# Performance work log

Measured on AMD Instinct MI355X. Metric: run time of the kernel, lower is better.

## Reference

```python
import jax, jax.numpy as jnp
import numpy as np

H = 4          # number of GCN heads (hard-coded self.h = 4)
EPS = 1e-6     # MWPToolkit LayerNorm eps
B, K, D, HID = 16, 1024, 256, 256
DK = D // H


def setup_inputs() -> dict:
    key = jax.random.key(0)
    ks = jax.random.split(key, 12)
    sc = lambda fan_in: 1.0 / np.sqrt(fan_in).astype(np.float32)
    return {
        "graph_nodes": jax.random.normal(ks[0], (B, K, D), jnp.float32),
        "graph": jax.random.randint(ks[1], (B, 5, K, K), 0, 2, jnp.int32),
        # per-head GCN layer 1: GraphConvolution(indim -> hiddim)
        "Wg1": jax.random.normal(ks[2], (H, D, HID), jnp.float32) * sc(D),
        "bg1": jax.random.normal(ks[3], (H, HID), jnp.float32) * sc(D),
        # per-head GCN layer 2: GraphConvolution(hiddim -> d_k)
        "Wg2": jax.random.normal(ks[4], (H, HID, DK), jnp.float32) * sc(HID),
        "bg2": jax.random.normal(ks[5], (H, DK), jnp.float32) * sc(HID),
        # PositionwiseFeedForward: Linear(indim,hiddim) -> ReLU -> Linear(hiddim,outdim)
        "Wf1": jax.random.normal(ks[6], (D, HID), jnp.float32) * sc(D),
        "bf1": jax.random.normal(ks[7], (HID,), jnp.float32) * sc(D),
        "Wf2": jax.random.normal(ks[8], (HID, D), jnp.float32) * sc(HID),
        "bf2": jax.random.normal(ks[9], (D,), jnp.float32) * sc(HID),
        # LayerNorm(outdim) affine params
        "ln_a": jnp.ones((D,), jnp.float32),
        "ln_b": jnp.zeros((D,), jnp.float32),
    }


def reference(graph_nodes, graph, Wg1, bg1, Wg2, bg2, Wf1, bf1, Wf2, bf2, ln_a, ln_b):
    adj = graph.astype(jnp.float32)                      # (B, 5, K, K)
    # adj_list = [adj[:,1], adj[:,1], adj[:,4], adj[:,4]] -> stack heads
    adj_h = jnp.stack([adj[:, 1], adj[:, 1], adj[:, 4], adj[:, 4]])  # (H,B,K,K)

    # GCN layer 1 (all heads at once): relu(adj @ (x @ W1) + b1)
    sup1 = jnp.einsum('bkd,hdf->hbkf', graph_nodes, Wg1)            # (H,B,K,HID)
    h1 = jax.nn.relu(jnp.einsum('hbkj,hbjf->hbkf', adj_h, sup1)
                     + bg1[:, None, None, :])
    # (dropout is identity in eval)
    # GCN layer 2: adj @ (h1 @ W2) + b2
    sup2 = jnp.einsum('hbkf,hfe->hbke', h1, Wg2)                    # (H,B,K,DK)
    h2 = jnp.einsum('hbkj,hbje->hbke', adj_h, sup2) + bg2[:, None, None, :]

    # concat heads along feature dim: (B,K,H*DK) == (B,K,D)
    g = jnp.transpose(h2, (1, 2, 0, 3)).reshape(h2.shape[1], h2.shape[2], -1)

    # MWPToolkit LayerNorm: a*(x-mean)/(std+eps)+b, std unbiased (ddof=1)
    mu = g.mean(-1, keepdims=True)
    sd = jnp.std(g, axis=-1, keepdims=True, ddof=1)
    g = ln_a * (g - mu) / (sd + EPS) + ln_b + graph_nodes           # residual

    # PositionwiseFeedForward + residual (dropout identity in eval)
    ff = jax.nn.relu(g @ Wf1 + bf1) @ Wf2 + bf2
    out = ff + g
    return adj, out
```

## Files before the change

kernel.cpp:

```cpp
#include <hip/hip_runtime.h>

typedef unsigned short ushort_t;
using short8  = __attribute__((ext_vector_type(8))) short;
using floatx4 = __attribute__((ext_vector_type(4))) float;

__device__ __forceinline__ ushort_t f2bf(float f) {
  unsigned int x = __builtin_bit_cast(unsigned int, f);
  x += 0x7fffu + ((x >> 16) & 1u);
  return (ushort_t)(x >> 16);
}

__device__ __forceinline__ void gld16(const ushort_t* g, ushort_t* l) {
  __builtin_amdgcn_global_load_lds(
      (const __attribute__((address_space(1))) void*)(unsigned long long)(uintptr_t)g,
      (__attribute__((address_space(3))) void*)l, 16, 0, 0);
}

template <typename F>
__device__ __forceinline__ void gemm_tile(const ushort_t* __restrict__ A, int lda,
                                          const ushort_t* __restrict__ BT, int ldb,
                                          int K, F epi) {
  __shared__ ushort_t As[128 * 64];
  __shared__ ushort_t Bs[128 * 64];

  const int tid  = threadIdx.x;
  const int wave = tid >> 6;
  const int lane = tid & 63;
  const int l15  = lane & 15;
  const int quad = lane >> 4;
  const int wm   = wave >> 1;
  const int wn   = wave & 1;

  const int srow8  = lane >> 3;
  const int schunk = lane & 7;
  const int gcol   = ((schunk ^ srow8) * 8);

  const ushort_t* gA = A  + (size_t)(wave * 32 + srow8) * lda + gcol;
  const ushort_t* gB = BT + (size_t)(wave * 32 + srow8) * ldb + gcol;
  ushort_t* lA = As + (wave * 32) * 64;
  ushort_t* lB = Bs + (wave * 32) * 64;

  floatx4 acc[4][4] = {};
  const int arow0 = (wm * 64 + l15) * 64;
  const int brow0 = (wn * 64 + l15) * 64;
  const int cx    = l15 & 7;

  for (int k0 = 0; k0 < K; k0 += 64) {
#pragma unroll
    for (int ci = 0; ci < 4; ci++) {
      gld16(gA + (size_t)(ci * 8) * lda, lA + ci * 512);
      gld16(gB + (size_t)(ci * 8) * ldb, lB + ci * 512);
    }
    gA += 64; gB += 64;
    __syncthreads();
#pragma unroll
    for (int ks = 0; ks < 2; ks++) {
      const int cs = ((ks * 4 + quad) ^ cx) * 8;
      short8 af[4], bfr[4];
#pragma unroll
      for (int i = 0; i < 4; i++) af[i]  = *(const short8*)(As + arow0 + i * 1024 + cs);
#pragma unroll
      for (int j = 0; j < 4; j++) bfr[j] = *(const short8*)(Bs + brow0 + j * 1024 + cs);
#pragma unroll
      for (int i = 0; i < 4; i++)
#pragma unroll
        for (int j = 0; j < 4; j++)
          acc[i][j] = __builtin_amdgcn_mfma_f32_16x16x32_bf16(af[i], bfr[j], acc[i][j], 0, 0, 0);
    }
    __syncthreads();
  }

#pragma unroll
  for (int i = 0; i < 4; i++)
#pragma unroll
    for (int j = 0; j < 4; j++)
#pragma unroll
      for (int r = 0; r < 4; r++)
        epi(wm * 64 + i * 16 + quad * 4 + r, wn * 64 + j * 16 + l15, acc[i][j][r]);
}

template <typename F>
__device__ __forceinline__ void gemm_tile64(const ushort_t* __restrict__ A, int lda,
                                            const ushort_t* __restrict__ BT, int ldb,
                                            int K, F epi) {
  __shared__ ushort_t As[64 * 64];
  __shared__ ushort_t Bs[128 * 64];

  const int tid  = threadIdx.x;
  const int wave = tid >> 6;
  const int lane = tid & 63;
  const int l15  = lane & 15;
  const int quad = lane >> 4;
  const int wm   = wave >> 1;
  const int wn   = wave & 1;

  const int srow8  = lane >> 3;
  const int schunk = lane & 7;
  const int gcol   = ((schunk ^ srow8) * 8);

  const ushort_t* gA = A  + (size_t)(wave * 16 + srow8) * lda + gcol;
  const ushort_t* gB = BT + (size_t)(wave * 32 + srow8) * ldb + gcol;
  ushort_t* lA = As + (wave * 16) * 64;
  ushort_t* lB = Bs + (wave * 32) * 64;

  floatx4 acc[2][4] = {};
  const int arow0 = (wm * 32 + l15) * 64;
  const int brow0 = (wn * 64 + l15) * 64;
  const int cx    = l15 & 7;

  for (int k0 = 0; k0 < K; k0 += 64) {
#pragma unroll
    for (int ci = 0; ci < 2; ci++)
      gld16(gA + (size_t)(ci * 8) * lda, lA + ci * 512);
#pragma unroll
    for (int ci = 0; ci < 4; ci++)
      gld16(gB + (size_t)(ci * 8) * ldb, lB + ci * 512);
    gA += 64; gB += 64;
    __syncthreads();
#pragma unroll
    for (int ks = 0; ks < 2; ks++) {
      const int cs = ((ks * 4 + quad) ^ cx) * 8;
      short8 af[2], bfr[4];
#pragma unroll
      for (int i = 0; i < 2; i++) af[i]  = *(const short8*)(As + arow0 + i * 1024 + cs);
#pragma unroll
      for (int j = 0; j < 4; j++) bfr[j] = *(const short8*)(Bs + brow0 + j * 1024 + cs);
#pragma unroll
      for (int i = 0; i < 2; i++)
#pragma unroll
        for (int j = 0; j < 4; j++)
          acc[i][j] = __builtin_amdgcn_mfma_f32_16x16x32_bf16(af[i], bfr[j], acc[i][j], 0, 0, 0);
    }
    __syncthreads();
  }

#pragma unroll
  for (int i = 0; i < 2; i++)
#pragma unroll
    for (int j = 0; j < 4; j++)
#pragma unroll
      for (int r = 0; r < 4; r++)
        epi(wm * 32 + i * 16 + quad * 4 + r, wn * 64 + j * 16 + l15, acc[i][j][r]);
}

__global__ __launch_bounds__(256) void k_prep(const int* __restrict__ graph,
                                              float* __restrict__ adj_out,
                                              ushort_t* __restrict__ adjb,
                                              const float* __restrict__ gn,
                                              ushort_t* __restrict__ XT,
                                              const float* __restrict__ Wg1, const float* __restrict__ Wg2,
                                              const float* __restrict__ Wf1, const float* __restrict__ Wf2,
                                              ushort_t* __restrict__ W1T, ushort_t* __restrict__ W2pT,
                                              ushort_t* __restrict__ Wf1T, ushort_t* __restrict__ Wf2T) {
  __shared__ float t[64][68];
  const int bid = blockIdx.x;
  if (bid < 81920) {
    const size_t i = (size_t)bid * 256 + threadIdx.x;
    int4 v = ((const int4*)graph)[i];
    float4 f = make_float4((float)v.x, (float)v.y, (float)v.z, (float)v.w);
    ((float4*)adj_out)[i] = f;
    const size_t e0 = i * 4;
    const unsigned sb = (unsigned)(e0 >> 20);
    const unsigned s = sb % 5u, b = sb / 5u;
    if (s == 1u || s == 4u) {
      const unsigned tt = (s == 4u) ? 1u : 0u;
      ushort4 h;
      h.x = f2bf(f.x); h.y = f2bf(f.y); h.z = f2bf(f.z); h.w = f2bf(f.w);
      *(ushort4*)(adjb + (((size_t)(b * 2 + tt)) << 20) + (e0 & 0xFFFFFu)) = h;
    }
  } else if (bid < 82944) {
    const int id = bid - 81920;
    const int kt = id & 15, dt = (id >> 4) & 3, b = id >> 6;
    const int r  = threadIdx.x >> 4;
    const int c4 = (threadIdx.x & 15) * 4;
#pragma unroll
    for (int rr = 0; rr < 4; rr++) {
      const int kl = rr * 16 + r;
      float4 v = *(const float4*)(gn + ((size_t)(b * 1024 + kt * 64 + kl)) * 256 + dt * 64 + c4);
      t[kl][c4] = v.x; t[kl][c4 + 1] = v.y; t[kl][c4 + 2] = v.z; t[kl][c4 + 3] = v.w;
    }
    __syncthreads();
#pragma unroll
    for (int rr = 0; rr < 4; rr++) {
      const int dl = rr * 16 + r;
      ushort4 h;
      h.x = f2bf(t[c4][dl]);     h.y = f2bf(t[c4 + 1][dl]);
      h.z = f2bf(t[c4 + 2][dl]); h.w = f2bf(t[c4 + 3][dl]);
      *(ushort4*)(XT + ((size_t)(b * 256 + dt * 64 + dl)) * 1024 + kt * 64 + c4) = h;
    }
  } else {
    const int i = (bid - 82944) * 256 + threadIdx.x;
    if (i < 262144) {
      const int fI = i >> 8, d = i & 255;
      const int h = fI >> 8, ff = fI & 255;
      W1T[i] = f2bf(Wg1[((h << 8) + d) * 256 + ff]);
    } else if (i < 393216) {
      const int j = i - 262144;
      const int tt = j >> 16, rem = j & 65535;
      const int ep = rem >> 9, k = rem & 511;
      const int hh = ep >> 6;
      const float v = ((k >> 8) == hh)
          ? Wg2[(((tt * 2 + hh) << 8) + (k & 255)) * 64 + (ep & 63)] : 0.f;
      W2pT[j] = f2bf(v);
    } else if (i < 458752) {
      const int j = i - 393216;
      const int n = j >> 8, k = j & 255;
      Wf1T[j] = f2bf(Wf1[k * 256 + n]);
    } else if (i < 524288) {
      const int j = i - 458752;
      const int n = j >> 8, k = j & 255;
      Wf2T[j] = f2bf(Wf2[k * 256 + n]);
    }
  }
}


__global__ __launch_bounds__(256) void k_ax(const ushort_t* __restrict__ adjb,
                                            const ushort_t* __restrict__ XT,
                                            ushort_t* __restrict__ AX) {
  const int nt = blockIdx.x, mt = blockIdx.y, bt = blockIdx.z;
  const int b = bt >> 1;
  const ushort_t* A  = adjb + ((size_t)bt << 20) + (size_t)mt * 128 * 1024;
  const ushort_t* BT = XT + ((size_t)b << 18) + (size_t)nt * 128 * 1024;
  ushort_t* C = AX + ((size_t)bt << 18);
  gemm_tile(A, 1024, BT, 1024, 1024, [&](int r, int c, float v) {
    C[(size_t)(mt * 128 + r) * 256 + nt * 128 + c] = f2bf(v);
  });
}

__global__ __launch_bounds__(256) void k_h1(const ushort_t* __restrict__ AX,
                                            const ushort_t* __restrict__ W1T,
                                            const float* __restrict__ bg1,
                                            ushort_t* __restrict__ h1) {
  const int nt = blockIdx.x, mt = blockIdx.y, b = blockIdx.z;
  const int t = nt >> 2;
  const ushort_t* A  = AX + ((size_t)(b * 2 + t) << 18) + (size_t)mt * 128 * 256;
  const ushort_t* BT = W1T + (size_t)nt * 128 * 256;
  ushort_t* C = h1 + ((size_t)b << 20);
  const float* bias = bg1 + nt * 128;
  gemm_tile(A, 256, BT, 256, 256, [&](int r, int c, float v) {
    C[(size_t)(mt * 128 + r) * 1024 + nt * 128 + c] = f2bf(fmaxf(v + bias[c], 0.f));
  });
}

__global__ __launch_bounds__(256) void k_g3(const ushort_t* __restrict__ W2pT,
                                            const ushort_t* __restrict__ h1,
                                            ushort_t* __restrict__ sup2T) {
  const int mx = blockIdx.x, nt = blockIdx.y, bt = blockIdx.z;
  const int b = bt >> 1, t = bt & 1;
  const ushort_t* A  = W2pT + (size_t)t * 65536 + (size_t)mx * 64 * 512;
  const ushort_t* BT = h1 + ((size_t)b << 20) + (size_t)nt * 131072 + t * 512;
  ushort_t* C = sup2T + (size_t)bt * 131072;
  gemm_tile64(A, 512, BT, 1024, 512, [&](int r, int c, float v) {
    C[(size_t)(mx * 64 + r) * 1024 + nt * 128 + c] = f2bf(v);
  });
}

__global__ __launch_bounds__(256) void k_tail(const ushort_t* __restrict__ adjb,
                                              const ushort_t* __restrict__ sup2T,
                                              const float* __restrict__ bg2,
                                              const float* __restrict__ gn,
                                              const float* __restrict__ la,
                                              const float* __restrict__ lb,
                                              const ushort_t* __restrict__ Wf1T,
                                              const float* __restrict__ bf1,
                                              const ushort_t* __restrict__ Wf2T,
                                              const float* __restrict__ bf2,
                                              float* __restrict__ out) {
  __shared__ ushort_t As[64 * 64];
  __shared__ ushort_t Bs[256 * 64];
  __shared__ ushort_t Ps[32 * 256];
  __shared__ ushort_t Ts[32 * 256];
  __shared__ float sred[4][32], qred[4][32];

  const int mt = blockIdx.x, b = blockIdx.y;
  const int tid = threadIdx.x, wave = tid >> 6, lane = tid & 63;
  const int l15 = lane & 15, quad = lane >> 4;
  const int wn = wave;
  const int tsel = wn >> 1;

  const int srow8 = lane >> 3, schunk = lane & 7;
  const int gcol = (schunk ^ srow8) * 8;

  const ushort_t* gA = adjb + ((size_t)(b * 2 + (wave >> 1)) << 20)
                     + (size_t)(mt * 32 + (wave & 1) * 16 + srow8) * 1024 + gcol;
  const ushort_t* gB = sup2T + (size_t)(b * 2 + (wave >> 1)) * 131072
                     + (size_t)((wave & 1) * 64 + srow8) * 1024 + gcol;
  ushort_t* lA = As + (wave * 16) * 64;
  ushort_t* lB = Bs + (wave * 64) * 64;

  floatx4 acc[2][4] = {};
  const int arow0 = (tsel * 32 + l15) * 64;
  const int brow0 = (wn * 64 + l15) * 64;
  const int cx = l15 & 7;

  for (int k0 = 0; k0 < 1024; k0 += 64) {
#pragma unroll
    for (int ci = 0; ci < 2; ci++)
      gld16(gA + (size_t)(ci * 8) * 1024, lA + ci * 512);
#pragma unroll
    for (int ci = 0; ci < 8; ci++)
      gld16(gB + (size_t)(ci * 8) * 1024, lB + ci * 512);
    gA += 64; gB += 64;
    __syncthreads();
#pragma unroll
    for (int ks = 0; ks < 2; ks++) {
      const int cs = ((ks * 4 + quad) ^ cx) * 8;
      short8 af[2], bfr[4];
#pragma unroll
      for (int i = 0; i < 2; i++) af[i]  = *(const short8*)(As + arow0 + i * 1024 + cs);
#pragma unroll
      for (int j = 0; j < 4; j++) bfr[j] = *(const short8*)(Bs + brow0 + j * 1024 + cs);
#pragma unroll
      for (int i = 0; i < 2; i++)
#pragma unroll
        for (int j = 0; j < 4; j++)
          acc[i][j] = __builtin_amdgcn_mfma_f32_16x16x32_bf16(af[i], bfr[j], acc[i][j], 0, 0, 0);
    }
    __syncthreads();
  }

  float laj[4], lbj[4];
#pragma unroll
  for (int j = 0; j < 4; j++) {
    const int colg = wn * 64 + j * 16 + l15;
    const float bj = bg2[colg];
    laj[j] = la[colg]; lbj[j] = lb[colg];
#pragma unroll
    for (int i = 0; i < 2; i++)
#pragma unroll
      for (int r = 0; r < 4; r++) acc[i][j][r] += bj;
  }
#pragma unroll
  for (int i = 0; i < 2; i++)
#pragma unroll
    for (int r = 0; r < 4; r++) {
      float s = 0.f, q = 0.f;
#pragma unroll
      for (int j = 0; j < 4; j++) { const float v = acc[i][j][r]; s += v; q += v * v; }
#pragma unroll
      for (int m = 1; m < 16; m <<= 1) { s += __shfl_xor(s, m); q += __shfl_xor(q, m); }
      if (l15 == 0) {
        const int row = i * 16 + quad * 4 + r;
        sred[wn][row] = s; qred[wn][row] = q;
      }
    }
  __syncthreads();

  const size_t rowbase = (size_t)(b * 1024 + mt * 32);
  float glnreg[2][4][4];
#pragma unroll
  for (int i = 0; i < 2; i++)
#pragma unroll
    for (int r = 0; r < 4; r++) {
      const int row = i * 16 + quad * 4 + r;
      const float S = sred[0][row] + sred[1][row] + sred[2][row] + sred[3][row];
      const float Q = qred[0][row] + qred[1][row] + qred[2][row] + qred[3][row];
      const float mu = S * (1.f / 256.f);
      const float var = fmaxf((Q - S * mu) * (1.f / 255.f), 0.f);
      const float inv = 1.f / (sqrtf(var) + 1e-6f);
      const float* gnr = gn + (rowbase + row) * 256;
#pragma unroll
      for (int j = 0; j < 4; j++) {
        const int colg = wn * 64 + j * 16 + l15;
        const float g = laj[j] * (acc[i][j][r] - mu) * inv + lbj[j] + gnr[colg];
        glnreg[i][j][r] = g;
        Ps[row * 256 + ((((colg >> 3) ^ row) & 31) << 3) + (colg & 7)] = f2bf(g);
      }
    }
  __syncthreads();

  floatx4 acc2[2][4] = {};
  for (int k0 = 0; k0 < 256; k0 += 64) {
#pragma unroll
    for (int ci = 0; ci < 8; ci++)
      gld16(Wf1T + (size_t)(wave * 64 + ci * 8 + srow8) * 256 + k0 + gcol,
            Bs + (wave * 64 + ci * 8) * 64);
    __syncthreads();
#pragma unroll
    for (int ks = 0; ks < 2; ks++) {
      const int c32 = (k0 >> 3) + ks * 4 + quad;
      const int cs = ((ks * 4 + quad) ^ cx) * 8;
      short8 af[2], bfr[4];
#pragma unroll
      for (int i = 0; i < 2; i++) {
        const int row = i * 16 + l15;
        af[i] = *(const short8*)(Ps + row * 256 + (((c32 ^ row) & 31) << 3));
      }
#pragma unroll
      for (int j = 0; j < 4; j++) bfr[j] = *(const short8*)(Bs + brow0 + j * 1024 + cs);
#pragma unroll
      for (int i = 0; i < 2; i++)
#pragma unroll
        for (int j = 0; j < 4; j++)
          acc2[i][j] = __builtin_amdgcn_mfma_f32_16x16x32_bf16(af[i], bfr[j], acc2[i][j], 0, 0, 0);
    }
    __syncthreads();
  }

#pragma unroll
  for (int j = 0; j < 4; j++) {
    const int colg = wn * 64 + j * 16 + l15;
    const float bj = bf1[colg];
#pragma unroll
    for (int i = 0; i < 2; i++)
#pragma unroll
      for (int r = 0; r < 4; r++) {
        const int row = i * 16 + quad * 4 + r;
        const float v = fmaxf(acc2[i][j][r] + bj, 0.f);
        Ts[row * 256 + ((((colg >> 3) ^ row) & 31) << 3) + (colg & 7)] = f2bf(v);
      }
  }
  __syncthreads();

  floatx4 acc3[2][4] = {};
  for (int k0 = 0; k0 < 256; k0 += 64) {
#pragma unroll
    for (int ci = 0; ci < 8; ci++)
      gld16(Wf2T + (size_t)(wave * 64 + ci * 8 + srow8) * 256 + k0 + gcol,
            Bs + (wave * 64 + ci * 8) * 64);
    __syncthreads();
#pragma unroll
    for (int ks = 0; ks < 2; ks++) {
      const int c32 = (k0 >> 3) + ks * 4 + quad;
      const int cs = ((ks * 4 + quad) ^ cx) * 8;
      short8 af[2], bfr[4];
#pragma unroll
      for (int i = 0; i < 2; i++) {
        const int row = i * 16 + l15;
        af[i] = *(const short8*)(Ts + row * 256 + (((c32 ^ row) & 31) << 3));
      }
#pragma unroll
      for (int j = 0; j < 4; j++) bfr[j] = *(const short8*)(Bs + brow0 + j * 1024 + cs);
#pragma unroll
      for (int i = 0; i < 2; i++)
#pragma unroll
        for (int j = 0; j < 4; j++)
          acc3[i][j] = __builtin_amdgcn_mfma_f32_16x16x32_bf16(af[i], bfr[j], acc3[i][j], 0, 0, 0);
    }
    __syncthreads();
  }

#pragma unroll
  for (int j = 0; j < 4; j++) {
    const int colg = wn * 64 + j * 16 + l15;
    const float bj = bf2[colg];
#pragma unroll
    for (int i = 0; i < 2; i++)
#pragma unroll
      for (int r = 0; r < 4; r++) {
        const int row = i * 16 + quad * 4 + r;
        out[(rowbase + row) * 256 + colg] = acc3[i][j][r] + bj + glnreg[i][j][r];
      }
  }
}

extern "C" void kernel_launch(void* const* d_in, const int* in_sizes, int n_in,
                              void* d_out, int out_size, void* d_ws, size_t ws_size,
                              hipStream_t stream) {
  const float* gnodes = (const float*)d_in[0];
  const int*   graph  = (const int*)d_in[1];
  const float* Wg1 = (const float*)d_in[2];
  const float* bg1 = (const float*)d_in[3];
  const float* Wg2 = (const float*)d_in[4];
  const float* bg2 = (const float*)d_in[5];
  const float* Wf1 = (const float*)d_in[6];
  const float* bf1 = (const float*)d_in[7];
  const float* Wf2 = (const float*)d_in[8];
  const float* bf2 = (const float*)d_in[9];
  const float* ln_a = (const float*)d_in[10];
  const float* ln_b = (const float*)d_in[11];

  float* adj_out = (float*)d_out;
  float* out     = (float*)d_out + 83886080;

  char* ws = (char*)d_ws;
  ushort_t* adjb  = (ushort_t*)(ws);
  ushort_t* XT    = (ushort_t*)(ws + 67108864);
  ushort_t* W1T   = (ushort_t*)(ws + 75497472);
  ushort_t* W2pT  = (ushort_t*)(ws + 76021760);
  ushort_t* Wf1T  = (ushort_t*)(ws + 76283904);
  ushort_t* Wf2T  = (ushort_t*)(ws + 76414976);
  ushort_t* AX    = (ushort_t*)(ws + 76546048);
  ushort_t* h1    = (ushort_t*)(ws + 93323264);
  ushort_t* sup2T = (ushort_t*)(ws + 126877696);

  k_prep<<<84992, 256, 0, stream>>>(graph, adj_out, adjb, gnodes, XT,
                                    Wg1, Wg2, Wf1, Wf2, W1T, W2pT, Wf1T, Wf2T);

  k_ax<<<dim3(2, 8, 32), 256, 0, stream>>>(adjb, XT, AX);
  k_h1<<<dim3(8, 8, 16), 256, 0, stream>>>(AX, W1T, bg1, h1);
  k_g3<<<dim3(2, 8, 32), 256, 0, stream>>>(W2pT, h1, sup2T);
  k_tail<<<dim3(32, 16), 256, 0, stream>>>(adjb, sup2T, bg2, gnodes, ln_a, ln_b,
                                           Wf1T, bf1, Wf2T, bf2, out);
}
```

Measured before the change: 665.0 us.

## Fuse adjacency-X, layer-1 GCN, and layer-2 support GEMMs into one kernel

Replaces the three separate GEMM kernels (adj@X, AX@W1 with bias and ReLU, W2@h1) with a single kernel. Each block computes a 64-row AX tile, keeps it in swizzled LDS, then loops over four 128-wide feature chunks, producing h1 in LDS and accumulating sup2 directly. This removes the global AX and h1 intermediates and two kernel launches. In exchange the grid is smaller (512 blocks), LDS use per block is higher, and the W1/W2 loads are not double-buffered.

Result: no change. 657.6 us (-1.1%).

```diff
diff --git a/kernel.cpp b/kernel.cpp
--- a/kernel.cpp
+++ b/kernel.cpp
@@ -14,133 +14,6 @@
   __builtin_amdgcn_global_load_lds(
       (const __attribute__((address_space(1))) void*)(unsigned long long)(uintptr_t)g,
       (__attribute__((address_space(3))) void*)l, 16, 0, 0);
-}
-
-template <typename F>
-__device__ __forceinline__ void gemm_tile(const ushort_t* __restrict__ A, int lda,
-                                          const ushort_t* __restrict__ BT, int ldb,
-                                          int K, F epi) {
-  __shared__ ushort_t As[128 * 64];
-  __shared__ ushort_t Bs[128 * 64];
-
-  const int tid  = threadIdx.x;
-  const int wave = tid >> 6;
-  const int lane = tid & 63;
-  const int l15  = lane & 15;
-  const int quad = lane >> 4;
-  const int wm   = wave >> 1;
-  const int wn   = wave & 1;
-
-  const int srow8  = lane >> 3;
-  const int schunk = lane & 7;
-  const int gcol   = ((schunk ^ srow8) * 8);
-
-  const ushort_t* gA = A  + (size_t)(wave * 32 + srow8) * lda + gcol;
-  const ushort_t* gB = BT + (size_t)(wave * 32 + srow8) * ldb + gcol;
-  ushort_t* lA = As + (wave * 32) * 64;
-  ushort_t* lB = Bs + (wave * 32) * 64;
-
-  floatx4 acc[4][4] = {};
-  const int arow0 = (wm * 64 + l15) * 64;
-  const int brow0 = (wn * 64 + l15) * 64;
-  const int cx    = l15 & 7;
-
-  for (int k0 = 0; k0 < K; k0 += 64) {
-#pragma unroll
-    for (int ci = 0; ci < 4; ci++) {
-      gld16(gA + (size_t)(ci * 8) * lda, lA + ci * 512);
-      gld16(gB + (size_t)(ci * 8) * ldb, lB + ci * 512);
-    }
-    gA += 64; gB += 64;
-    __syncthreads();
-#pragma unroll
-    for (int ks = 0; ks < 2; ks++) {
-      const int cs = ((ks * 4 + quad) ^ cx) * 8;
-      short8 af[4], bfr[4];
-#pragma unroll
-      for (int i = 0; i < 4; i++) af[i]  = *(const short8*)(As + arow0 + i * 1024 + cs);
-#pragma unroll
-      for (int j = 0; j < 4; j++) bfr[j] = *(const short8*)(Bs + brow0 + j * 1024 + cs);
-#pragma unroll
-      for (int i = 0; i < 4; i++)
-#pragma unroll
-        for (int j = 0; j < 4; j++)
-          acc[i][j] = __builtin_amdgcn_mfma_f32_16x16x32_bf16(af[i], bfr[j], acc[i][j], 0, 0, 0);
-    }
-    __syncthreads();
-  }
-
-#pragma unroll
-  for (int i = 0; i < 4; i++)
-#pragma unroll
-    for (int j = 0; j < 4; j++)
-#pragma unroll
-      for (int r = 0; r < 4; r++)
-        epi(wm * 64 + i * 16 + quad * 4 + r, wn * 64 + j * 16 + l15, acc[i][j][r]);
-}
-
-template <typename F>
-__device__ __forceinline__ void gemm_tile64(const ushort_t* __restrict__ A, int lda,
-                                            const ushort_t* __restrict__ BT, int ldb,
-                                            int K, F epi) {
-  __shared__ ushort_t As[64 * 64];
-  __shared__ ushort_t Bs[128 * 64];
-
-  const int tid  = threadIdx.x;
-  const int wave = tid >> 6;
-  const int lane = tid & 63;
-  const int l15  = lane & 15;
-  const int quad = lane >> 4;
-  const int wm   = wave >> 1;
-  const int wn   = wave & 1;
-
-  const int srow8  = lane >> 3;
-  const int schunk = lane & 7;
-  const int gcol   = ((schunk ^ srow8) * 8);
-
-  const ushort_t* gA = A  + (size_t)(wave * 16 + srow8) * lda + gcol;
-  const ushort_t* gB = BT + (size_t)(wave * 32 + srow8) * ldb + gcol;
-  ushort_t* lA = As + (wave * 16) * 64;
-  ushort_t* lB = Bs + (wave * 32) * 64;
-
-  floatx4 acc[2][4] = {};
-  const int arow0 = (wm * 32 + l15) * 64;
-  const int brow0 = (wn * 64 + l15) * 64;
-  const int cx    = l15 & 7;
-
-  for (int k0 = 0; k0 < K; k0 += 64) {
-#pragma unroll
-    for (int ci = 0; ci < 2; ci++)
-      gld16(gA + (size_t)(ci * 8) * lda, lA + ci * 512);
-#pragma unroll
-    for (int ci = 0; ci < 4; ci++)
-      gld16(gB + (size_t)(ci * 8) * ldb, lB + ci * 512);
-    gA += 64; gB += 64;
-    __syncthreads();
-#pragma unroll
-    for (int ks = 0; ks < 2; ks++) {
-      const int cs = ((ks * 4 + quad) ^ cx) * 8;
-      short8 af[2], bfr[4];
-#pragma unroll
-      for (int i = 0; i < 2; i++) af[i]  = *(const short8*)(As + arow0 + i * 1024 + cs);
-#pragma unroll
-      for (int j = 0; j < 4; j++) bfr[j] = *(const short8*)(Bs + brow0 + j * 1024 + cs);
-#pragma unroll
-      for (int i = 0; i < 2; i++)
-#pragma unroll
-        for (int j = 0; j < 4; j++)
-          acc[i][j] = __builtin_amdgcn_mfma_f32_16x16x32_bf16(af[i], bfr[j], acc[i][j], 0, 0, 0);
-    }
-    __syncthreads();
-  }
-
-#pragma unroll
-  for (int i = 0; i < 2; i++)
-#pragma unroll
-    for (int j = 0; j < 4; j++)
-#pragma unroll
-      for (int r = 0; r < 4; r++)
-        epi(wm * 32 + i * 16 + quad * 4 + r, wn * 64 + j * 16 + l15, acc[i][j][r]);
 }
 
 __global__ __launch_bounds__(256) void k_prep(const int* __restrict__ graph,
@@ -214,46 +87,160 @@
   }
 }
 
-
-__global__ __launch_bounds__(256) void k_ax(const ushort_t* __restrict__ adjb,
-                                            const ushort_t* __restrict__ XT,
-                                            ushort_t* __restrict__ AX) {
-  const int nt = blockIdx.x, mt = blockIdx.y, bt = blockIdx.z;
-  const int b = bt >> 1;
-  const ushort_t* A  = adjb + ((size_t)bt << 20) + (size_t)mt * 128 * 1024;
-  const ushort_t* BT = XT + ((size_t)b << 18) + (size_t)nt * 128 * 1024;
-  ushort_t* C = AX + ((size_t)bt << 18);
-  gemm_tile(A, 1024, BT, 1024, 1024, [&](int r, int c, float v) {
-    C[(size_t)(mt * 128 + r) * 256 + nt * 128 + c] = f2bf(v);
-  });
-}
-
-__global__ __launch_bounds__(256) void k_h1(const ushort_t* __restrict__ AX,
-                                            const ushort_t* __restrict__ W1T,
-                                            const float* __restrict__ bg1,
-                                            ushort_t* __restrict__ h1) {
-  const int nt = blockIdx.x, mt = blockIdx.y, b = blockIdx.z;
-  const int t = nt >> 2;
-  const ushort_t* A  = AX + ((size_t)(b * 2 + t) << 18) + (size_t)mt * 128 * 256;
-  const ushort_t* BT = W1T + (size_t)nt * 128 * 256;
-  ushort_t* C = h1 + ((size_t)b << 20);
-  const float* bias = bg1 + nt * 128;
-  gemm_tile(A, 256, BT, 256, 256, [&](int r, int c, float v) {
-    C[(size_t)(mt * 128 + r) * 1024 + nt * 128 + c] = f2bf(fmaxf(v + bias[c], 0.f));
-  });
-}
-
-__global__ __launch_bounds__(256) void k_g3(const ushort_t* __restrict__ W2pT,
-                                            const ushort_t* __restrict__ h1,
-                                            ushort_t* __restrict__ sup2T) {
-  const int mx = blockIdx.x, nt = blockIdx.y, bt = blockIdx.z;
+__global__ __launch_bounds__(256) void k_mid(const ushort_t* __restrict__ adjb,
+                                             const ushort_t* __restrict__ XT,
+                                             const ushort_t* __restrict__ W1T,
+                                             const float* __restrict__ bg1,
+                                             const ushort_t* __restrict__ W2pT,
+                                             ushort_t* __restrict__ sup2T) {
+  __shared__ ushort_t As[64 * 64];
+  __shared__ ushort_t Bs[256 * 64];
+  __shared__ ushort_t AXs[64 * 256];
+  ushort_t* Hs = Bs + 8192;
+
+  const int mt = blockIdx.x, bt = blockIdx.y;
   const int b = bt >> 1, t = bt & 1;
-  const ushort_t* A  = W2pT + (size_t)t * 65536 + (size_t)mx * 64 * 512;
-  const ushort_t* BT = h1 + ((size_t)b << 20) + (size_t)nt * 131072 + t * 512;
-  ushort_t* C = sup2T + (size_t)bt * 131072;
-  gemm_tile64(A, 512, BT, 1024, 512, [&](int r, int c, float v) {
-    C[(size_t)(mx * 64 + r) * 1024 + nt * 128 + c] = f2bf(v);
-  });
+  const int tid = threadIdx.x, wave = tid >> 6, lane = tid & 63;
+  const int l15 = lane & 15, quad = lane >> 4;
+  const int wm = wave >> 1, wn = wave & 1;
+  const int srow8 = lane >> 3, schunk = lane & 7;
+  const int gcol = (schunk ^ srow8) * 8;
+  const int cx = l15 & 7;
+
+  const ushort_t* gA = adjb + ((size_t)bt << 20) + (size_t)(mt * 64 + wave * 16 + srow8) * 1024 + gcol;
+  const ushort_t* gB = XT + ((size_t)b << 18) + (size_t)(wave * 64 + srow8) * 1024 + gcol;
+  ushort_t* lA = As + (wave * 16) * 64;
+  ushort_t* lB = Bs + (wave * 64) * 64;
+
+  floatx4 acc1[2][8] = {};
+  const int arow1 = (wm * 32 + l15) * 64;
+  const int brow1 = (wn * 128 + l15) * 64;
+
+  for (int k0 = 0; k0 < 1024; k0 += 64) {
+#pragma unroll
+    for (int ci = 0; ci < 2; ci++) gld16(gA + (size_t)(ci * 8) * 1024, lA + ci * 512);
+#pragma unroll
+    for (int ci = 0; ci < 8; ci++) gld16(gB + (size_t)(ci * 8) * 1024, lB + ci * 512);
+    gA += 64; gB += 64;
+    __syncthreads();
+#pragma unroll
+    for (int ks = 0; ks < 2; ks++) {
+      const int cs = ((ks * 4 + quad) ^ cx) * 8;
+      short8 af[2], bfr[8];
+#pragma unroll
+      for (int i = 0; i < 2; i++) af[i]  = *(const short8*)(As + arow1 + i * 1024 + cs);
+#pragma unroll
+      for (int j = 0; j < 8; j++) bfr[j] = *(const short8*)(Bs + brow1 + j * 1024 + cs);
+#pragma unroll
+      for (int i = 0; i < 2; i++)
+#pragma unroll
+        for (int j = 0; j < 8; j++)
+          acc1[i][j] = __builtin_amdgcn_mfma_f32_16x16x32_bf16(af[i], bfr[j], acc1[i][j], 0, 0, 0);
+    }
+    __syncthreads();
+  }
+
+#pragma unroll
+  for (int i = 0; i < 2; i++)
+#pragma unroll
+    for (int j = 0; j < 8; j++)
+#pragma unroll
+      for (int r = 0; r < 4; r++) {
+        const int row = wm * 32 + i * 16 + quad * 4 + r;
+        const int d   = wn * 128 + j * 16 + l15;
+        AXs[row * 256 + ((((d >> 3) ^ row) & 31) << 3) + (d & 7)] = f2bf(acc1[i][j][r]);
+      }
+  __syncthreads();
+
+  floatx4 acc4[4][2] = {};
+
+#pragma unroll 1
+  for (int nn = 0; nn < 4; nn++) {
+    const int fg = t * 512 + nn * 128;
+
+    floatx4 acc3[2][4] = {};
+    for (int k0 = 0; k0 < 256; k0 += 64) {
+#pragma unroll
+      for (int ci = 0; ci < 4; ci++)
+        gld16(W1T + (size_t)(fg + wave * 32 + ci * 8 + srow8) * 256 + k0 + gcol,
+              Bs + (wave * 32 + ci * 8) * 64);
+      __syncthreads();
+#pragma unroll
+      for (int ks = 0; ks < 2; ks++) {
+        const int c32 = (k0 >> 3) + ks * 4 + quad;
+        const int cs = ((ks * 4 + quad) ^ cx) * 8;
+        short8 af[2], bfr[4];
+#pragma unroll
+        for (int i = 0; i < 2; i++) {
+          const int row = wm * 32 + i * 16 + l15;
+          af[i] = *(const short8*)(AXs + row * 256 + (((c32 ^ row) & 31) << 3));
+        }
+#pragma unroll
+        for (int j = 0; j < 4; j++)
+          bfr[j] = *(const short8*)(Bs + (wn * 64 + j * 16 + l15) * 64 + cs);
+#pragma unroll
+        for (int i = 0; i < 2; i++)
+#pragma unroll
+          for (int j = 0; j < 4; j++)
+            acc3[i][j] = __builtin_amdgcn_mfma_f32_16x16x32_bf16(af[i], bfr[j], acc3[i][j], 0, 0, 0);
+      }
+      __syncthreads();
+    }
+
+#pragma unroll
+    for (int j = 0; j < 4; j++) {
+      const int fl = wn * 64 + j * 16 + l15;
+      const float bj = bg1[fg + fl];
+#pragma unroll
+      for (int i = 0; i < 2; i++)
+#pragma unroll
+        for (int r = 0; r < 4; r++) {
+          const int row = wm * 32 + i * 16 + quad * 4 + r;
+          const float v = fmaxf(acc3[i][j][r] + bj, 0.f);
+          Hs[row * 128 + ((((fl >> 3) ^ row) & 15) << 3) + (fl & 7)] = f2bf(v);
+        }
+    }
+    __syncthreads();
+
+    for (int k0 = 0; k0 < 128; k0 += 64) {
+#pragma unroll
+      for (int ci = 0; ci < 4; ci++)
+        gld16(W2pT + (size_t)t * 65536 + (size_t)(wave * 32 + ci * 8 + srow8) * 512 + nn * 128 + k0 + gcol,
+              Bs + (wave * 32 + ci * 8) * 64);
+      __syncthreads();
+#pragma unroll
+      for (int ks = 0; ks < 2; ks++) {
+        const int c32h = (k0 >> 3) + ks * 4 + quad;
+        const int cs = ((ks * 4 + quad) ^ cx) * 8;
+        short8 af[4], bfr[2];
+#pragma unroll
+        for (int i = 0; i < 4; i++)
+          af[i] = *(const short8*)(Bs + (wm * 64 + i * 16 + l15) * 64 + cs);
+#pragma unroll
+        for (int j = 0; j < 2; j++) {
+          const int row = wn * 32 + j * 16 + l15;
+          bfr[j] = *(const short8*)(Hs + row * 128 + (((c32h ^ row) & 15) << 3));
+        }
+#pragma unroll
+        for (int i = 0; i < 4; i++)
+#pragma unroll
+          for (int j = 0; j < 2; j++)
+            acc4[i][j] = __builtin_amdgcn_mfma_f32_16x16x32_bf16(af[i], bfr[j], acc4[i][j], 0, 0, 0);
+      }
+      __syncthreads();
+    }
+  }
+
+#pragma unroll
+  for (int i = 0; i < 4; i++)
+#pragma unroll
+    for (int j = 0; j < 2; j++)
+#pragma unroll
+      for (int r = 0; r < 4; r++) {
+        const int ep = wm * 64 + i * 16 + quad * 4 + r;
+        const int kp = mt * 64 + wn * 32 + j * 16 + l15;
+        sup2T[(size_t)bt * 131072 + (size_t)ep * 1024 + kp] = f2bf(acc4[i][j][r]);
+      }
 }
 
 __global__ __launch_bounds__(256) void k_tail(const ushort_t* __restrict__ adjb,
@@ -481,16 +468,13 @@
   ushort_t* W2pT  = (ushort_t*)(ws + 76021760);
   ushort_t* Wf1T  = (ushort_t*)(ws + 76283904);
   ushort_t* Wf2T  = (ushort_t*)(ws + 76414976);
-  ushort_t* AX    = (ushort_t*)(ws + 76546048);
-  ushort_t* h1    = (ushort_t*)(ws + 93323264);
-  ushort_t* sup2T = (ushort_t*)(ws + 126877696);
+  ushort_t* sup2T = (ushort_t*)(ws + 76546048);
 
   k_prep<<<84992, 256, 0, stream>>>(graph, adj_out, adjb, gnodes, XT,
                                     Wg1, Wg2, Wf1, Wf2, W1T, W2pT, Wf1T, Wf2T);
 
-  k_ax<<<dim3(2, 8, 32), 256, 0, stream>>>(adjb, XT, AX);
-  k_h1<<<dim3(8, 8, 16), 256, 0, stream>>>(AX, W1T, bg1, h1);
-  k_g3<<<dim3(2, 8, 32), 256, 0, stream>>>(W2pT, h1, sup2T);
+  k_mid<<<dim3(16, 32), 256, 0, stream>>>(adjb, XT, W1T, bg1, W2pT, sup2T);
+
   k_tail<<<dim3(32, 16), 256, 0, stream>>>(adjb, sup2T, bg2, gnodes, ln_a, ln_b,
                                            Wf1T, bf1, Wf2T, bf2, out);
 }
```
